# Kernel tuning notes

Measured on AMD Instinct MI355X. Metric: run time of the kernel, lower is better.

## Reference

```python
import jax, jax.numpy as jnp
import numpy as np
import math

N_HEADS = 16

def setup_inputs() -> dict:
    key = jax.random.key(0)
    ks = jax.random.split(key, 5)
    B, S, D = 4, 2048, 1024
    scale = 0.02
    return {
        "x": jax.random.normal(ks[0], (B, S, D), dtype=jnp.float32),
        "w_in": jax.random.normal(ks[1], (D, 3 * D), dtype=jnp.float32) * scale,
        "b_in": jax.random.normal(ks[2], (3 * D,), dtype=jnp.float32) * scale,
        "w_out": jax.random.normal(ks[3], (D, D), dtype=jnp.float32) * scale,
        "b_out": jax.random.normal(ks[4], (D,), dtype=jnp.float32) * scale,
    }

def reference(x, w_in, b_in, w_out, b_out):
    B, S, D = x.shape
    H = N_HEADS
    dh = D // H
    qkv = x @ w_in + b_in                      # [B,S,3D]
    q, k, v = jnp.split(qkv, 3, axis=-1)
    # [B,S,D] -> [B,H,S,dh]
    q = q.reshape(B, S, H, dh).transpose(0, 2, 1, 3)
    k = k.reshape(B, S, H, dh).transpose(0, 2, 1, 3)
    v = v.reshape(B, S, H, dh).transpose(0, 2, 1, 3)
    scores = jnp.einsum("bhqd,bhkd->bhqk", q, k) / math.sqrt(dh)
    causal = jnp.tril(jnp.ones((S, S), dtype=bool))  # allow k <= q
    scores = jnp.where(causal, scores, -jnp.inf)
    wei = jax.nn.softmax(scores, axis=-1)
    out = jnp.einsum("bhqk,bhkd->bhqd", wei, v)      # [B,H,S,dh]
    out = out.transpose(0, 2, 1, 3).reshape(B, S, D)
    return out @ w_out + b_out
```

## Files before the change

kernel.cpp:

```cpp
#include <hip/hip_runtime.h>

typedef unsigned short u16;
typedef unsigned int   u32;
typedef float  f32x4  __attribute__((ext_vector_type(4)));
typedef __bf16 bf16x8 __attribute__((ext_vector_type(8)));
typedef __bf16 bf16x4 __attribute__((ext_vector_type(4)));
typedef short  s16x4  __attribute__((ext_vector_type(4)));
typedef unsigned short u16x8 __attribute__((ext_vector_type(8)));
typedef unsigned int   u32x4 __attribute__((ext_vector_type(4)));

__device__ __forceinline__ u16 f2bf(float f) {
  u32 u = __builtin_bit_cast(u32, f);
  u = (u + 0x7fffu + ((u >> 16) & 1u)) >> 16;
  return (u16)u;
}

__device__ __forceinline__ void gload_lds16(const void* g, void* l) {
  __builtin_amdgcn_global_load_lds(
      (const __attribute__((address_space(1))) void*)g,
      (__attribute__((address_space(3))) void*)l, 16, 0, 0);
}

__global__ __launch_bounds__(256) void conv_f32_bf16(
    const float* __restrict__ in, u16* __restrict__ out, int n8) {
  int i = blockIdx.x * 256 + threadIdx.x;
  if (i >= n8) return;
  const float4* p = (const float4*)in;
  float4 a = p[2 * i], b = p[2 * i + 1];
  u16x8 r;
  r[0] = f2bf(a.x); r[1] = f2bf(a.y); r[2] = f2bf(a.z); r[3] = f2bf(a.w);
  r[4] = f2bf(b.x); r[5] = f2bf(b.y); r[6] = f2bf(b.z); r[7] = f2bf(b.w);
  ((u16x8*)out)[i] = r;
}

__global__ __launch_bounds__(256) void conv_transpose(
    const float* __restrict__ in, u16* __restrict__ out, int K, int N) {
  __shared__ float tile[64][65];
  int nb = N >> 6;
  int tk = blockIdx.x / nb, tn = blockIdx.x % nb;
  int t = threadIdx.x;
  int kl = t >> 4, n4 = (t & 15) * 4;
#pragma unroll
  for (int i = 0; i < 4; ++i) {
    int k = kl + 16 * i;
    float4 v = *(const float4*)(in + (size_t)(tk * 64 + k) * N + tn * 64 + n4);
    tile[k][n4] = v.x; tile[k][n4 + 1] = v.y; tile[k][n4 + 2] = v.z; tile[k][n4 + 3] = v.w;
  }
  __syncthreads();
  int nl = t >> 4, k4 = (t & 15) * 4;
#pragma unroll
  for (int i = 0; i < 4; ++i) {
    int n = nl + 16 * i;
    ushort4 o;
    o.x = f2bf(tile[k4 + 0][n]); o.y = f2bf(tile[k4 + 1][n]);
    o.z = f2bf(tile[k4 + 2][n]); o.w = f2bf(tile[k4 + 3][n]);
    *(ushort4*)(out + (size_t)(tn * 64 + n) * K + tk * 64 + k4) = o;
  }
}

template <int OUT_BF16, int SCALE_Q>
__global__ __launch_bounds__(256, 2) void gemm_kernel(
    const u16* __restrict__ A, const u16* __restrict__ Bt,
    const float* __restrict__ bias, void* __restrict__ C,
    int M, int N, int K) {
  __shared__ __align__(16) char smem[32768];
  char* As = smem;
  char* Bs = smem + 16384;
  int tid = threadIdx.x, w = tid >> 6, lane = tid & 63;
  int g = lane >> 4, l15 = lane & 15, l7 = lane & 7;
  int cpx = (int)gridDim.x >> 3;
  int bid = (blockIdx.x & 7) * cpx + (blockIdx.x >> 3);
  int nblk = N >> 7;
  int bm = bid / nblk, bn = bid % nblk;
  int m0 = bm << 7, n0 = bn << 7;
  int wm = w >> 1, wn = w & 1;

  f32x4 acc[4][4];
#pragma unroll
  for (int i = 0; i < 4; ++i)
#pragma unroll
    for (int j = 0; j < 4; ++j) acc[i][j] = f32x4{0.f, 0.f, 0.f, 0.f};

  int kiter = K >> 6;
  for (int kt = 0; kt < kiter; ++kt) {
    __syncthreads();
#pragma unroll
    for (int i = 0; i < 4; ++i) {
      int rbase = 32 * w + 8 * i;
      int row = rbase + (lane >> 3);
      int koff = kt * 64 + 8 * (l7 ^ (row & 7));
      gload_lds16(A + (size_t)(m0 + row) * K + koff, As + rbase * 128);
      gload_lds16(Bt + (size_t)(n0 + row) * K + koff, Bs + rbase * 128);
    }
    __syncthreads();
#pragma unroll
    for (int ks = 0; ks < 2; ++ks) {
      bf16x8 af[4], bf[4];
#pragma unroll
      for (int mi = 0; mi < 4; ++mi) {
        int ml = wm * 64 + mi * 16 + l15;
        af[mi] = *(const bf16x8*)(As + ml * 128 + ((ks * 64 + g * 16) ^ ((ml & 7) << 4)));
      }
#pragma unroll
      for (int ni = 0; ni < 4; ++ni) {
        int nl = wn * 64 + ni * 16 + l15;
        bf[ni] = *(const bf16x8*)(Bs + nl * 128 + ((ks * 64 + g * 16) ^ ((nl & 7) << 4)));
      }
#pragma unroll
      for (int mi = 0; mi < 4; ++mi)
#pragma unroll
        for (int ni = 0; ni < 4; ++ni)
          acc[mi][ni] = __builtin_amdgcn_mfma_f32_16x16x32_bf16(af[mi], bf[ni], acc[mi][ni], 0, 0, 0);
    }
  }

#pragma unroll
  for (int ni = 0; ni < 4; ++ni) {
    int col = n0 + wn * 64 + ni * 16 + l15;
    float bv = bias[col];
    float sc = (SCALE_Q && col < 1024) ? 0.18033688011112042f : 1.0f;
#pragma unroll
    for (int mi = 0; mi < 4; ++mi) {
      int rowb = m0 + wm * 64 + mi * 16 + g * 4;
#pragma unroll
      for (int r = 0; r < 4; ++r) {
        float v = (acc[mi][ni][r] + bv) * sc;
        if (OUT_BF16)
          ((u16*)C)[(size_t)(rowb + r) * N + col] = f2bf(v);
        else
          ((float*)C)[(size_t)(rowb + r) * N + col] = v;
      }
    }
  }
}


#if __has_builtin(__builtin_amdgcn_mfma_f32_16x16x16bf16_1k)
#define HAVE_MFMA16 1
__device__ __forceinline__ f32x4 mfma16(s16x4 a, s16x4 b, f32x4 c) {
  return __builtin_amdgcn_mfma_f32_16x16x16bf16_1k(a, b, c, 0, 0, 0);
}
#endif

struct V2reg { u16x8 a, b; };

__device__ __forceinline__ void stage_k(const u16* qb, char* kbuf, int kvt,
                                        int h, int w, int lane) {
  int l7 = lane & 7;
#pragma unroll
  for (int i = 0; i < 2; ++i) {
    int rbase = w * 16 + i * 8;
    int row = rbase + (lane >> 3);
    const u16* src = qb + (size_t)(kvt * 64 + row) * 3072 + 1024 + h * 64 + 8 * (l7 ^ (row & 7));
    gload_lds16(src, kbuf + rbase * 128);
  }
}

__device__ __forceinline__ V2reg load_v(const u16* qb, int kvt, int h, int kv0, int d0) {
  const u16* vs = qb + (size_t)(kvt * 64 + kv0) * 3072 + 2048 + h * 64 + d0;
  V2reg r;
  r.a = *(const u16x8*)vs;
  r.b = *(const u16x8*)(vs + 3072);
  return r;
}

__device__ __forceinline__ void write_v(char* vbuf, V2reg v, int kv0, int d0) {
#pragma unroll
  for (int j = 0; j < 8; ++j) {
    int d = d0 + j;
    u32 val = (u32)v.a[j] | ((u32)v.b[j] << 16);
    int sw = ((d & 7) ^ (d >> 3)) << 4;
    *(u32*)(vbuf + d * 128 + ((2 * kv0) ^ sw)) = val;
  }
}

__global__ __launch_bounds__(256, 4) void attn_fwd(
    const u16* __restrict__ qkv, u16* __restrict__ aout) {
  const int S = 2048, D3 = 3072;
  int bh = blockIdx.x & 63;
  int qt = 31 - (blockIdx.x >> 6);
  int b = bh >> 4, h = bh & 15;
  const u16* qb = qkv + (size_t)b * S * D3;

  int tid = threadIdx.x;
  int w = tid >> 6, lane = tid & 63;
  int g = lane >> 4, l15 = lane & 15, l7 = lane & 7;

  __shared__ __align__(16) char Kb[2][8192];
  __shared__ __align__(16) char Vb[2][8192];

  int qrow = qt * 64 + w * 16 + l15;
  const u16* qp = qb + (size_t)qrow * D3 + h * 64 + g * 8;
  bf16x8 qf0 = *(const bf16x8*)qp;
  bf16x8 qf1 = *(const bf16x8*)(qp + 32);

  f32x4 oaT[4];
#pragma unroll
  for (int i = 0; i < 4; ++i) oaT[i] = f32x4{0.f, 0.f, 0.f, 0.f};
  f32x4 l_acc = {0.f, 0.f, 0.f, 0.f};
  float m_s = -3e38f;

  int vkv0 = w * 16 + ((lane >> 3) << 1);
  int vd0 = l7 * 8;

  stage_k(qb, Kb[0], 0, h, w, lane);
  {
    V2reg v = load_v(qb, 0, h, vkv0, vd0);
    write_v(Vb[0], v, vkv0, vd0);
  }
  __syncthreads();

  V2reg vreg;
  for (int kvt = 0; kvt <= qt; ++kvt) {
    int cur = kvt & 1;
    if (kvt < qt) {
      stage_k(qb, Kb[cur ^ 1], kvt + 1, h, w, lane);
      vreg = load_v(qb, kvt + 1, h, vkv0, vd0);
    }

    f32x4 sT[4];
    __builtin_amdgcn_s_setprio(1);
#pragma unroll
    for (int nb = 0; nb < 4; ++nb) {
      int kv = nb * 16 + l15;
      const char* kb = Kb[cur] + kv * 128;
      int sw = (kv & 7) << 4;
      bf16x8 kf0 = *(const bf16x8*)(kb + ((g * 16) ^ sw));
      bf16x8 kf1 = *(const bf16x8*)(kb + ((64 + g * 16) ^ sw));
      f32x4 z = {0.f, 0.f, 0.f, 0.f};
      z = __builtin_amdgcn_mfma_f32_16x16x32_bf16(kf0, qf0, z, 0, 0, 0);
      z = __builtin_amdgcn_mfma_f32_16x16x32_bf16(kf1, qf1, z, 0, 0, 0);
      sT[nb] = z;
    }
    __builtin_amdgcn_s_setprio(0);

    if (kvt == qt) {
      int qloc = w * 16 + l15;
#pragma unroll
      for (int nb = 0; nb < 4; ++nb)
#pragma unroll
        for (int r = 0; r < 4; ++r)
          if (nb * 16 + g * 4 + r > qloc) sT[nb][r] = -1e30f;
    }

    float pm = -3e38f;
#pragma unroll
    for (int nb = 0; nb < 4; ++nb)
#pragma unroll
      for (int r = 0; r < 4; ++r) pm = fmaxf(pm, sT[nb][r]);
    pm = fmaxf(pm, __shfl_xor(pm, 16));
    pm = fmaxf(pm, __shfl_xor(pm, 32));
    if (!__all(pm - m_s <= 8.0f)) {
      float newm = fmaxf(m_s, pm);
      float corr = __builtin_amdgcn_exp2f(m_s - newm);
      m_s = newm;
      l_acc[0] *= corr;
#pragma unroll
      for (int db = 0; db < 4; ++db)
#pragma unroll
        for (int r = 0; r < 4; ++r) oaT[db][r] *= corr;
    }
#pragma unroll
    for (int nb = 0; nb < 4; ++nb)
#pragma unroll
      for (int r = 0; r < 4; ++r)
        sT[nb][r] = __builtin_amdgcn_exp2f(sT[nb][r] - m_s);

#ifdef HAVE_MFMA16
    s16x4 pf[4];
#pragma unroll
    for (int nb = 0; nb < 4; ++nb) {
      bf16x4 t;
#pragma unroll
      for (int r = 0; r < 4; ++r) t[r] = (__bf16)sT[nb][r];
      pf[nb] = __builtin_bit_cast(s16x4, t);
    }
    s16x4 ones;
#pragma unroll
    for (int r = 0; r < 4; ++r) ones[r] = (short)0x3F80;
    __builtin_amdgcn_s_setprio(1);
#pragma unroll
    for (int nb = 0; nb < 4; ++nb) l_acc = mfma16(ones, pf[nb], l_acc);
#pragma unroll
    for (int db = 0; db < 4; ++db) {
      int d = db * 16 + l15;
      const char* vb = Vb[cur] + d * 128;
      int swd = ((d & 7) ^ (d >> 3)) << 4;
#pragma unroll
      for (int nb = 0; nb < 4; ++nb) {
        bf16x4 vf = *(const bf16x4*)(vb + ((nb * 32 + g * 8) ^ swd));
        oaT[db] = mfma16(__builtin_bit_cast(s16x4, vf), pf[nb], oaT[db]);
      }
    }
    __builtin_amdgcn_s_setprio(0);
#else
    u32 wlo[4], whi[4];
#pragma unroll
    for (int nb = 0; nb < 4; ++nb) {
      wlo[nb] = (u32)f2bf(sT[nb][0]) | ((u32)f2bf(sT[nb][1]) << 16);
      whi[nb] = (u32)f2bf(sT[nb][2]) | ((u32)f2bf(sT[nb][3]) << 16);
    }
    int srcA = (2 * (g & 1)) * 16 + l15;
    int srcB = srcA + 16;
    bool hi = (g >> 1) != 0;
    bf16x8 ones8;
#pragma unroll
    for (int j = 0; j < 8; ++j) ones8[j] = __builtin_bit_cast(__bf16, (u16)0x3F80);
    __builtin_amdgcn_s_setprio(1);
#pragma unroll
    for (int kb2 = 0; kb2 < 2; ++kb2) {
      int nbE = kb2 * 2, nbO = kb2 * 2 + 1;
      u32 a0 = __shfl(wlo[nbE], srcA), a1 = __shfl(whi[nbE], srcA);
      u32 a2 = __shfl(wlo[nbE], srcB), a3 = __shfl(whi[nbE], srcB);
      u32 b0 = __shfl(wlo[nbO], srcA), b1 = __shfl(whi[nbO], srcA);
      u32 b2 = __shfl(wlo[nbO], srcB), b3 = __shfl(whi[nbO], srcB);
      u32x4 ow = {hi ? b0 : a0, hi ? b1 : a1, hi ? b2 : a2, hi ? b3 : a3};
      bf16x8 pfrag = __builtin_bit_cast(bf16x8, ow);
      l_acc = __builtin_amdgcn_mfma_f32_16x16x32_bf16(ones8, pfrag, l_acc, 0, 0, 0);
#pragma unroll
      for (int db = 0; db < 4; ++db) {
        int d = db * 16 + l15;
        int swd = ((d & 7) ^ (d >> 3)) << 4;
        bf16x8 vf = *(const bf16x8*)(Vb[cur] + d * 128 + ((kb2 * 64 + g * 16) ^ swd));
        oaT[db] = __builtin_amdgcn_mfma_f32_16x16x32_bf16(vf, pfrag, oaT[db], 0, 0, 0);
      }
    }
    __builtin_amdgcn_s_setprio(0);
#endif

    if (kvt < qt) {
      write_v(Vb[cur ^ 1], vreg, vkv0, vd0);
      __syncthreads();
    }
  }

  float inv = 1.0f / l_acc[0];
  size_t obase = (size_t)(b * S + qt * 64 + w * 16 + l15) * 1024 + h * 64;
#pragma unroll
  for (int db = 0; db < 4; ++db) {
    ushort4 st;
    st.x = f2bf(oaT[db][0] * inv);
    st.y = f2bf(oaT[db][1] * inv);
    st.z = f2bf(oaT[db][2] * inv);
    st.w = f2bf(oaT[db][3] * inv);
    *(ushort4*)(aout + obase + db * 16 + g * 4) = st;
  }
}

extern "C" void kernel_launch(void* const* d_in, const int* in_sizes, int n_in,
                              void* d_out, int out_size, void* d_ws, size_t ws_size,
                              hipStream_t stream) {
  (void)in_sizes; (void)n_in; (void)out_size;
  const float* x     = (const float*)d_in[0];
  const float* w_in  = (const float*)d_in[1];
  const float* b_in  = (const float*)d_in[2];
  const float* w_out = (const float*)d_in[3];
  const float* b_out = (const float*)d_in[4];
  float* out = (float*)d_out;
  char* ws = (char*)d_ws;
  if (ws_size < 92274688u) return;

  u16* xb     = (u16*)(ws);
  u16* w_inT  = (u16*)(ws + (16u << 20));
  u16* w_outT = (u16*)(ws + (22u << 20));
  u16* qkv    = (u16*)(ws + (24u << 20));
  u16* aout   = (u16*)(ws + (72u << 20));

  conv_f32_bf16<<<4096, 256, 0, stream>>>(x, xb, 1048576);
  conv_transpose<<<768, 256, 0, stream>>>(w_in, w_inT, 1024, 3072);
  conv_transpose<<<256, 256, 0, stream>>>(w_out, w_outT, 1024, 1024);
  gemm_kernel<1, 1><<<1536, 256, 0, stream>>>(xb, w_inT, b_in, qkv, 8192, 3072, 1024);
  attn_fwd<<<2048, 256, 0, stream>>>(qkv, aout);
  gemm_kernel<0, 0><<<512, 256, 0, stream>>>(aout, w_outT, b_out, out, 8192, 1024, 1024);
}
```

Measured before the change: 259.2 us.

## Replace GEMM with 8-wave 256x128 tile, double-buffered LDS prefetch pipeline

Rewrites both projection GEMMs as a 512-thread kernel with 256x128 output tiles and two LDS buffers. Global-to-LDS loads for tile t+2 are issued in quarters, interleaved between MFMA groups and ordered with explicit vmcnt/lgkmcnt waits and raw barriers. s_setprio raises wave priority around the MFMA bursts. The goal is to hide global load latency and cut the per-iteration double __syncthreads stalls, at the cost of 96KB LDS per block and more fragile hand-managed synchronisation.

Result: no change. 262.3 us (+1.2%).

```diff
diff --git a/kernel.cpp b/kernel.cpp
--- a/kernel.cpp
+++ b/kernel.cpp
@@ -20,6 +20,10 @@
       (const __attribute__((address_space(1))) void*)g,
       (__attribute__((address_space(3))) void*)l, 16, 0, 0);
 }
+
+#define LGKM0()  asm volatile("s_waitcnt lgkmcnt(0)" ::: "memory")
+#define VMCNT6() asm volatile("s_waitcnt vmcnt(6)" ::: "memory")
+#define VMCNT0() asm volatile("s_waitcnt vmcnt(0)" ::: "memory")
 
 __global__ __launch_bounds__(256) void conv_f32_bf16(
     const float* __restrict__ in, u16* __restrict__ out, int n8) {
@@ -59,78 +63,142 @@
 }
 
 template <int OUT_BF16, int SCALE_Q>
-__global__ __launch_bounds__(256, 2) void gemm_kernel(
+__global__ __launch_bounds__(512, 2) void gemm8p(
     const u16* __restrict__ A, const u16* __restrict__ Bt,
     const float* __restrict__ bias, void* __restrict__ C,
     int M, int N, int K) {
-  __shared__ __align__(16) char smem[32768];
-  char* As = smem;
-  char* Bs = smem + 16384;
+  __shared__ __align__(16) char smem[2][49152];
   int tid = threadIdx.x, w = tid >> 6, lane = tid & 63;
-  int g = lane >> 4, l15 = lane & 15, l7 = lane & 7;
+  int g = lane >> 4, l15 = lane & 15, l7 = lane & 7, l8 = lane >> 3;
+  int wm = w >> 2, wn = w & 3;
   int cpx = (int)gridDim.x >> 3;
   int bid = (blockIdx.x & 7) * cpx + (blockIdx.x >> 3);
   int nblk = N >> 7;
   int bm = bid / nblk, bn = bid % nblk;
-  int m0 = bm << 7, n0 = bn << 7;
-  int wm = w >> 1, wn = w & 1;
-
-  f32x4 acc[4][4];
-#pragma unroll
-  for (int i = 0; i < 4; ++i)
-#pragma unroll
-    for (int j = 0; j < 4; ++j) acc[i][j] = f32x4{0.f, 0.f, 0.f, 0.f};
-
-  int kiter = K >> 6;
-  for (int kt = 0; kt < kiter; ++kt) {
-    __syncthreads();
-#pragma unroll
-    for (int i = 0; i < 4; ++i) {
-      int rbase = 32 * w + 8 * i;
-      int row = rbase + (lane >> 3);
-      int koff = kt * 64 + 8 * (l7 ^ (row & 7));
-      gload_lds16(A + (size_t)(m0 + row) * K + koff, As + rbase * 128);
-      gload_lds16(Bt + (size_t)(n0 + row) * K + koff, Bs + rbase * 128);
-    }
-    __syncthreads();
-#pragma unroll
-    for (int ks = 0; ks < 2; ++ks) {
-      bf16x8 af[4], bf[4];
-#pragma unroll
-      for (int mi = 0; mi < 4; ++mi) {
-        int ml = wm * 64 + mi * 16 + l15;
-        af[mi] = *(const bf16x8*)(As + ml * 128 + ((ks * 64 + g * 16) ^ ((ml & 7) << 4)));
-      }
-#pragma unroll
-      for (int ni = 0; ni < 4; ++ni) {
-        int nl = wn * 64 + ni * 16 + l15;
-        bf[ni] = *(const bf16x8*)(Bs + nl * 128 + ((ks * 64 + g * 16) ^ ((nl & 7) << 4)));
-      }
-#pragma unroll
-      for (int mi = 0; mi < 4; ++mi)
-#pragma unroll
-        for (int ni = 0; ni < 4; ++ni)
-          acc[mi][ni] = __builtin_amdgcn_mfma_f32_16x16x32_bf16(af[mi], bf[ni], acc[mi][ni], 0, 0, 0);
-    }
-  }
-
-#pragma unroll
-  for (int ni = 0; ni < 4; ++ni) {
-    int col = n0 + wn * 64 + ni * 16 + l15;
+  int m0 = bm << 8, n0 = bn << 7;
+
+  auto stageA = [&](int buf, int kt, int h) {
+#pragma unroll
+    for (int i = 0; i < 2; ++i) {
+      int row = h * 128 + w * 16 + i * 8 + l8;
+      const u16* src = A + (size_t)(m0 + row) * K + kt * 64 + 8 * (l7 ^ (row & 7));
+      gload_lds16(src, &smem[buf][(h * 128 + w * 16 + i * 8) * 128]);
+    }
+  };
+  auto stageB = [&](int buf, int kt, int h) {
+    int row = h * 64 + w * 8 + l8;
+    const u16* src = Bt + (size_t)(n0 + row) * K + kt * 64 + 8 * (l7 ^ (row & 7));
+    gload_lds16(src, &smem[buf][32768 + (h * 64 + w * 8) * 128]);
+  };
+  auto ldA = [&](int buf, int mh, int mi, int kk) -> bf16x8 {
+    int row = mh * 128 + wm * 64 + mi * 16 + l15;
+    return *(const bf16x8*)&smem[buf][row * 128 + (((kk * 4 + g) * 16) ^ ((row & 7) << 4))];
+  };
+  auto ldB = [&](int buf, int nh, int kk) -> bf16x8 {
+    int row = nh * 64 + wn * 16 + l15;
+    return *(const bf16x8*)&smem[buf][32768 + row * 128 + (((kk * 4 + g) * 16) ^ ((row & 7) << 4))];
+  };
+
+  f32x4 acc[2][4][2];
+#pragma unroll
+  for (int mh = 0; mh < 2; ++mh)
+#pragma unroll
+    for (int mi = 0; mi < 4; ++mi)
+#pragma unroll
+      for (int nh = 0; nh < 2; ++nh) acc[mh][mi][nh] = f32x4{0.f, 0.f, 0.f, 0.f};
+
+  const int NT = K >> 6;
+#pragma unroll
+  for (int t = 0; t < 2; ++t) {
+    stageB(t, t, 0); stageA(t, t, 0); stageB(t, t, 1); stageA(t, t, 1);
+  }
+  VMCNT6();
+  __builtin_amdgcn_s_barrier();
+
+  for (int t = 0; t < NT; ++t) {
+    int b = t & 1;
+    bool pf = (t + 2) < NT;
+    bf16x8 af[4][2], b0f[2], b1f[2];
+
+#pragma unroll
+    for (int mi = 0; mi < 4; ++mi)
+#pragma unroll
+      for (int kk = 0; kk < 2; ++kk) af[mi][kk] = ldA(b, 0, mi, kk);
+#pragma unroll
+    for (int kk = 0; kk < 2; ++kk) b0f[kk] = ldB(b, 0, kk);
+    LGKM0();
+    __builtin_amdgcn_s_barrier();
+    if (pf) stageB(b, t + 2, 0);
+    __builtin_amdgcn_s_setprio(1);
+#pragma unroll
+    for (int mi = 0; mi < 4; ++mi)
+#pragma unroll
+      for (int kk = 0; kk < 2; ++kk)
+        acc[0][mi][0] = __builtin_amdgcn_mfma_f32_16x16x32_bf16(af[mi][kk], b0f[kk], acc[0][mi][0], 0, 0, 0);
+    __builtin_amdgcn_s_setprio(0);
+
+#pragma unroll
+    for (int kk = 0; kk < 2; ++kk) b1f[kk] = ldB(b, 1, kk);
+    LGKM0();
+    __builtin_amdgcn_s_barrier();
+    if (pf) stageA(b, t + 2, 0);
+    __builtin_amdgcn_s_setprio(1);
+#pragma unroll
+    for (int mi = 0; mi < 4; ++mi)
+#pragma unroll
+      for (int kk = 0; kk < 2; ++kk)
+        acc[0][mi][1] = __builtin_amdgcn_mfma_f32_16x16x32_bf16(af[mi][kk], b1f[kk], acc[0][mi][1], 0, 0, 0);
+    __builtin_amdgcn_s_setprio(0);
+
+#pragma unroll
+    for (int mi = 0; mi < 4; ++mi)
+#pragma unroll
+      for (int kk = 0; kk < 2; ++kk) af[mi][kk] = ldA(b, 1, mi, kk);
+    LGKM0();
+    __builtin_amdgcn_s_barrier();
+    if (pf) stageB(b, t + 2, 1);
+    __builtin_amdgcn_s_setprio(1);
+#pragma unroll
+    for (int mi = 0; mi < 4; ++mi)
+#pragma unroll
+      for (int kk = 0; kk < 2; ++kk)
+        acc[1][mi][1] = __builtin_amdgcn_mfma_f32_16x16x32_bf16(af[mi][kk], b1f[kk], acc[1][mi][1], 0, 0, 0);
+    __builtin_amdgcn_s_setprio(0);
+
+    if (pf) stageA(b, t + 2, 1);
+    __builtin_amdgcn_s_setprio(1);
+#pragma unroll
+    for (int mi = 0; mi < 4; ++mi)
+#pragma unroll
+      for (int kk = 0; kk < 2; ++kk)
+        acc[1][mi][0] = __builtin_amdgcn_mfma_f32_16x16x32_bf16(af[mi][kk], b0f[kk], acc[1][mi][0], 0, 0, 0);
+    __builtin_amdgcn_s_setprio(0);
+
+    if (t < NT - 1) {
+      if (pf) VMCNT6(); else VMCNT0();
+      __builtin_amdgcn_s_barrier();
+    }
+  }
+
+#pragma unroll
+  for (int nh = 0; nh < 2; ++nh) {
+    int col = n0 + nh * 64 + wn * 16 + l15;
     float bv = bias[col];
     float sc = (SCALE_Q && col < 1024) ? 0.18033688011112042f : 1.0f;
 #pragma unroll
-    for (int mi = 0; mi < 4; ++mi) {
-      int rowb = m0 + wm * 64 + mi * 16 + g * 4;
-#pragma unroll
-      for (int r = 0; r < 4; ++r) {
-        float v = (acc[mi][ni][r] + bv) * sc;
-        if (OUT_BF16)
-          ((u16*)C)[(size_t)(rowb + r) * N + col] = f2bf(v);
-        else
-          ((float*)C)[(size_t)(rowb + r) * N + col] = v;
+    for (int mh = 0; mh < 2; ++mh)
+#pragma unroll
+      for (int mi = 0; mi < 4; ++mi) {
+        int rowb = m0 + mh * 128 + wm * 64 + mi * 16 + g * 4;
+#pragma unroll
+        for (int r = 0; r < 4; ++r) {
+          float v = (acc[mh][mi][nh][r] + bv) * sc;
+          if (OUT_BF16)
+            ((u16*)C)[(size_t)(rowb + r) * N + col] = f2bf(v);
+          else
+            ((float*)C)[(size_t)(rowb + r) * N + col] = v;
+        }
       }
-    }
   }
 }
 
@@ -369,7 +437,7 @@
   conv_f32_bf16<<<4096, 256, 0, stream>>>(x, xb, 1048576);
   conv_transpose<<<768, 256, 0, stream>>>(w_in, w_inT, 1024, 3072);
   conv_transpose<<<256, 256, 0, stream>>>(w_out, w_outT, 1024, 1024);
-  gemm_kernel<1, 1><<<1536, 256, 0, stream>>>(xb, w_inT, b_in, qkv, 8192, 3072, 1024);
+  gemm8p<1, 1><<<768, 512, 0, stream>>>(xb, w_inT, b_in, qkv, 8192, 3072, 1024);
   attn_fwd<<<2048, 256, 0, stream>>>(qkv, aout);
-  gemm_kernel<0, 0><<<512, 256, 0, stream>>>(aout, w_outT, b_out, out, 8192, 1024, 1024);
-}
+  gemm8p<0, 0><<<256, 512, 0, stream>>>(aout, w_outT, b_out, out, 8192, 1024, 1024);
+}
```
